# Optimization experiments

Measured on AMD Instinct MI355X. Metric: run time of the kernel, lower is better.

Reference implementation:

```python
import jax, jax.numpy as jnp
import numpy as np

N_NODES = 100000
N_EDGES = 800000
IN_FEAT = 64
HID_FEAT = 64
NUM_CLASS = 16


def _gcn_layer(H, src, dst, W, b, n_nodes):
    # Undirected aggregation: sum neighbor features in both edge directions,
    # plus self-loop, then linear transform.
    agg = (H
           + jax.ops.segment_sum(H[src], dst, num_segments=n_nodes)
           + jax.ops.segment_sum(H[dst], src, num_segments=n_nodes))
    return agg @ W + b


def setup_inputs() -> dict:
    key = jax.random.key(0)
    ks = jax.random.split(key, 8)
    X = jax.random.normal(ks[0], (N_NODES, IN_FEAT), dtype=jnp.float32)
    edge_list = jax.random.randint(ks[1], (2, N_EDGES), 0, N_NODES, dtype=jnp.int32)
    scale = 0.05
    W0 = jax.random.normal(ks[2], (IN_FEAT, HID_FEAT), dtype=jnp.float32) * scale
    W1 = jax.random.normal(ks[3], (HID_FEAT, HID_FEAT), dtype=jnp.float32) * scale
    W2 = jax.random.normal(ks[4], (HID_FEAT, HID_FEAT), dtype=jnp.float32) * scale
    W3 = jax.random.normal(ks[5], (HID_FEAT, NUM_CLASS), dtype=jnp.float32) * scale
    b0 = jnp.zeros((HID_FEAT,), jnp.float32)
    b1 = jnp.zeros((HID_FEAT,), jnp.float32)
    b2 = jnp.zeros((HID_FEAT,), jnp.float32)
    b3 = jnp.zeros((NUM_CLASS,), jnp.float32)
    return {"X": X, "edge_list": edge_list,
            "W0": W0, "b0": b0, "W1": W1, "b1": b1,
            "W2": W2, "b2": b2, "W3": W3, "b3": b3}


def reference(X, edge_list, W0, b0, W1, b1, W2, b2, W3, b3):
    n_nodes = X.shape[0]
    src, dst = edge_list[0], edge_list[1]
    # init layer + ReLU
    H = jax.nn.relu(_gcn_layer(X, src, dst, W0, b0, n_nodes))
    # 2 hidden layers + ReLU
    H = jax.nn.relu(_gcn_layer(H, src, dst, W1, b1, n_nodes))
    H = jax.nn.relu(_gcn_layer(H, src, dst, W2, b2, n_nodes))
    # output layer (no activation)
    H_out = _gcn_layer(H, src, dst, W3, b3, n_nodes)
    # global mean pooling over nodes -> [1, num_class]
    return jnp.mean(H_out, axis=0, keepdims=True)
```

## Files before the change

kernel.cpp:

```cpp
#include <hip/hip_runtime.h>

#define N_NODES 100000
#define N_EDGES 800000
#define SCAN_BLK 256
#define NB 391
#define NPB 256
#define CAP 5120
#define BIN_CAP 40
#define EDGES_PER_BLK 2048
#define BIN_GRID ((N_EDGES + EDGES_PER_BLK - 1) / EDGES_PER_BLK)

typedef unsigned int uint32;
typedef float f2x __attribute__((ext_vector_type(2)));

#if __has_builtin(__builtin_amdgcn_cvt_pk_f32_fp8) && __has_builtin(__builtin_amdgcn_cvt_pk_fp8_f32)
#define HW_FP8 1
#endif

__device__ __forceinline__ float fp8_dec_sw(uint32 v) {
    uint32 s = (v & 0x80u) << 24;
    uint32 e = (v >> 3) & 0xFu;
    uint32 m = v & 7u;
    if (e == 0) {
        float f = (float)m * 0.001953125f;
        return (v & 0x80u) ? -f : f;
    }
    return __uint_as_float(s | ((e + 120u) << 23) | (m << 20));
}
__device__ __forceinline__ uint32 fp8_enc_sw(float f) {
    uint32 u = __float_as_uint(f);
    uint32 s = (u >> 24) & 0x80u;
    uint32 a = u & 0x7FFFFFFFu;
    if (a < 0x3C000000u) {
        float af = __uint_as_float(a);
        uint32 m = (uint32)(af * 512.0f + 0.5f);
        if (m > 7u) return s | 0x08u;
        return s | m;
    }
    if (a >= 0x43E00000u) return s | 0x7Eu;
    uint32 r = a + 0x000FFFFFu + ((a >> 20) & 1u);
    uint32 e = (r >> 23) - 120u;
    uint32 m = (r >> 20) & 7u;
    if (e > 15u) return s | 0x7Eu;
    return s | (e << 3) | m;
}

__device__ __forceinline__ void dec4(uint32 v, float* o) {
#ifdef HW_FP8
    f2x lo = __builtin_amdgcn_cvt_pk_f32_fp8((int)v, false);
    f2x hi = __builtin_amdgcn_cvt_pk_f32_fp8((int)v, true);
    o[0] = lo.x; o[1] = lo.y; o[2] = hi.x; o[3] = hi.y;
#else
    o[0] = fp8_dec_sw(v); o[1] = fp8_dec_sw(v >> 8);
    o[2] = fp8_dec_sw(v >> 16); o[3] = fp8_dec_sw(v >> 24);
#endif
}
__device__ __forceinline__ uint32 enc4(float a, float b, float c, float d) {
#ifdef HW_FP8
    int v = 0;
    v = __builtin_amdgcn_cvt_pk_fp8_f32(a, b, v, false);
    v = __builtin_amdgcn_cvt_pk_fp8_f32(c, d, v, true);
    return (uint32)v;
#else
    return fp8_enc_sw(a) | (fp8_enc_sw(b) << 8) | (fp8_enc_sw(c) << 16) | (fp8_enc_sw(d) << 24);
#endif
}
__device__ __forceinline__ void acc16(uint4 h, float* a) {
    float t[16];
    dec4(h.x, t + 0); dec4(h.y, t + 4); dec4(h.z, t + 8); dec4(h.w, t + 12);
#pragma unroll
    for (int j = 0; j < 16; ++j) a[j] += t[j];
}

__global__ void f32_to_fp8_k(const float4* __restrict__ in, uint4* __restrict__ out, int n16) {
    int i = blockIdx.x * blockDim.x + threadIdx.x;
    if (i >= n16) return;
    float4 a = in[4 * i + 0];
    float4 b = in[4 * i + 1];
    float4 c = in[4 * i + 2];
    float4 d = in[4 * i + 3];
    uint4 o;
    o.x = enc4(a.x, a.y, a.z, a.w);
    o.y = enc4(b.x, b.y, b.z, b.w);
    o.z = enc4(c.x, c.y, c.z, c.w);
    o.w = enc4(d.x, d.y, d.z, d.w);
    out[i] = o;
}

__global__ void zero_int(int* __restrict__ p, int n) {
    int i = blockIdx.x * blockDim.x + threadIdx.x;
    if (i < n) p[i] = 0;
}

__global__ void zero_kernel(float* __restrict__ p, int n) {
    int i = blockIdx.x * blockDim.x + threadIdx.x;
    if (i < n) p[i] = 0.f;
}

__global__ void bin_kernel(const int* __restrict__ src, const int* __restrict__ dst,
                           int* __restrict__ bcnt, uint32* __restrict__ bpairs) {
    __shared__ int lcnt[NB];
    __shared__ uint32 lbin[NB * BIN_CAP];
    for (int b = threadIdx.x; b < NB; b += 256) lcnt[b] = 0;
    __syncthreads();

    int base = blockIdx.x * EDGES_PER_BLK;
#pragma unroll
    for (int j = 0; j < EDGES_PER_BLK / 256; ++j) {
        int e = base + j * 256 + threadIdx.x;
        if (e < N_EDGES) {
            int s = src[e], d = dst[e];
            {
                int b = d >> 8;
                uint32 val = ((uint32)(d & 255) << 17) | (uint32)s;
                int pos = atomicAdd(&lcnt[b], 1);
                if (pos < BIN_CAP) lbin[b * BIN_CAP + pos] = val;
                else {
                    int g = atomicAdd(&bcnt[b], 1);
                    if (g < CAP) bpairs[(size_t)b * CAP + g] = val;
                }
            }
            {
                int b = s >> 8;
                uint32 val = ((uint32)(s & 255) << 17) | (uint32)d;
                int pos = atomicAdd(&lcnt[b], 1);
                if (pos < BIN_CAP) lbin[b * BIN_CAP + pos] = val;
                else {
                    int g = atomicAdd(&bcnt[b], 1);
                    if (g < CAP) bpairs[(size_t)b * CAP + g] = val;
                }
            }
        }
    }
    __syncthreads();

    for (int b = threadIdx.x; b < NB; b += 256) {
        int k = lcnt[b];
        if (k > BIN_CAP) k = BIN_CAP;
        int g = 0;
        if (k > 0) g = atomicAdd(&bcnt[b], k);
        lcnt[b] = (g << 6) | k;
    }
    __syncthreads();
    const int TOT = NB * BIN_CAP;
    for (int idx = threadIdx.x; idx < TOT; idx += 256) {
        int b = idx / BIN_CAP;
        int j = idx - b * BIN_CAP;
        int pkv = lcnt[b];
        int k = pkv & 63;
        if (j < k) {
            int gg = (pkv >> 6) + j;
            if (gg < CAP) bpairs[(size_t)b * CAP + gg] = lbin[b * BIN_CAP + j];
        }
    }
}

__global__ void hist_kernel(const int* __restrict__ bcnt, const uint32* __restrict__ bpairs,
                            int* __restrict__ deg, int* __restrict__ partial) {
    __shared__ int h[NPB];
    int b = blockIdx.x;
    int t = threadIdx.x;
    h[t] = 0;
    __syncthreads();
    int cnt = bcnt[b];
    if (cnt > CAP) cnt = CAP;
    for (int i = t; i < cnt; i += 256)
        atomicAdd(&h[bpairs[(size_t)b * CAP + i] >> 17], 1);
    __syncthreads();
    int node = (b << 8) + t;
    int myh = h[t];
    if (node < N_NODES) deg[node] = myh;
    __syncthreads();
    for (int off = 128; off > 0; off >>= 1) {
        if (t < off) h[t] += h[t + off];
        __syncthreads();
    }
    if (t == 0) partial[b] = h[0];
}

__global__ void scan_tops(const int* __restrict__ partial, int* __restrict__ blockoff) {
    __shared__ int part[512];
    int t = threadIdx.x;
    part[t] = (t < NB) ? partial[t] : 0;
    __syncthreads();
    for (int off = 1; off < 512; off <<= 1) {
        int v = (t >= off) ? part[t - off] : 0;
        __syncthreads();
        part[t] += v;
        __syncthreads();
    }
    if (t < NB) blockoff[t] = (t == 0) ? 0 : part[t - 1];
}

__global__ void scan_apply(const int* __restrict__ deg, const int* __restrict__ blockoff,
                           int* __restrict__ rowptr) {
    __shared__ int part[SCAN_BLK];
    int t = threadIdx.x;
    int i = blockIdx.x * SCAN_BLK + t;
    int v = (i < N_NODES) ? deg[i] : 0;
    part[t] = v;
    __syncthreads();
    for (int off = 1; off < SCAN_BLK; off <<= 1) {
        int u = (t >= off) ? part[t - off] : 0;
        __syncthreads();
        part[t] += u;
        __syncthreads();
    }
    if (i < N_NODES) {
        int excl = blockoff[blockIdx.x] + part[t] - v;
        rowptr[i] = excl;
        if (i == N_NODES - 1) rowptr[N_NODES] = 2 * N_EDGES;
    }
}

__global__ void scatter_kernel(const int* __restrict__ bcnt, const uint32* __restrict__ bpairs,
                               const int* __restrict__ rowptr, int* __restrict__ adj) {
    __shared__ int lcur[NPB];
    __shared__ int stage[CAP];
    int b = blockIdx.x, t = threadIdx.x;
    int lo = b << 8;
    int base = rowptr[lo];
    int node = lo + t;
    lcur[t] = (node < N_NODES) ? (rowptr[node] - base) : 0;
    __syncthreads();
    int cnt = bcnt[b];
    if (cnt > CAP) cnt = CAP;
    for (int i = t; i < cnt; i += 256) {
        uint32 p = bpairs[(size_t)b * CAP + i];
        int ln = (int)(p >> 17);
        int nbr = (int)(p & 0x1FFFFu);
        int slot = atomicAdd(&lcur[ln], 1);
        if (slot < CAP) stage[slot] = nbr;
    }
    __syncthreads();
    for (int i = t; i < cnt; i += 256) adj[base + i] = stage[i];
}

#define FMA4(ACC, WV) ACC.x += a * (WV).x; ACC.y += a * (WV).y; \
                      ACC.z += a * (WV).z; ACC.w += a * (WV).w;
__global__ void __launch_bounds__(256)
fused_layer(const uint4* __restrict__ Hin,
            const int* __restrict__ rowptr,
            const int* __restrict__ adj,
            const float* __restrict__ W,
            const float* __restrict__ bias,
            uint4* __restrict__ Hout) {
    __shared__ uint4 aggL[64 * 5];

    int node_base = blockIdx.x * 64;
    {
        int n = node_base + (threadIdx.x >> 2);
        int c = threadIdx.x & 3;
        int ln = threadIdx.x >> 2;
        if (n < N_NODES) {
            int beg = rowptr[n], end = rowptr[n + 1];
            float a[16];
            uint4 s = Hin[(size_t)n * 4 + c];
            dec4(s.x, a + 0); dec4(s.y, a + 4); dec4(s.z, a + 8); dec4(s.w, a + 12);
            int i = beg;
            for (; i + 2 <= end; i += 2) {
                int v0 = adj[i];
                int v1 = adj[i + 1];
                uint4 h0 = Hin[(size_t)v0 * 4 + c];
                uint4 h1 = Hin[(size_t)v1 * 4 + c];
                acc16(h0, a);
                acc16(h1, a);
            }
            if (i < end) {
                uint4 h = Hin[(size_t)adj[i] * 4 + c];
                acc16(h, a);
            }
            uint4 o;
            o.x = enc4(a[0], a[1], a[2], a[3]);
            o.y = enc4(a[4], a[5], a[6], a[7]);
            o.z = enc4(a[8], a[9], a[10], a[11]);
            o.w = enc4(a[12], a[13], a[14], a[15]);
            aggL[ln * 5 + c] = o;
        }
    }
    __syncthreads();

    int ln2 = threadIdx.x & 63;
    int c2 = __builtin_amdgcn_readfirstlane(threadIdx.x >> 6);
    int n2 = node_base + ln2;
    if (n2 >= N_NODES) return;

    float4 acc0, acc1, acc2, acc3;
    {
        const float4* b4 = (const float4*)bias + c2 * 4;
        acc0 = b4[0]; acc1 = b4[1]; acc2 = b4[2]; acc3 = b4[3];
    }
    const float4* Wc = (const float4*)(W + c2 * 16);
#pragma unroll
    for (int q = 0; q < 4; ++q) {
        uint4 v = aggL[ln2 * 5 + q];
        float af[16];
        dec4(v.x, af + 0); dec4(v.y, af + 4); dec4(v.z, af + 8); dec4(v.w, af + 12);
#pragma unroll
        for (int k = 0; k < 16; ++k) {
            const float4* wr = Wc + (q * 16 + k) * 16;
            float a = af[k];
            float4 w0 = wr[0], w1 = wr[1], w2 = wr[2], w3 = wr[3];
            FMA4(acc0, w0)
            FMA4(acc1, w1)
            FMA4(acc2, w2)
            FMA4(acc3, w3)
        }
    }

    uint4 o;
    o.x = enc4(fmaxf(acc0.x, 0.f), fmaxf(acc0.y, 0.f), fmaxf(acc0.z, 0.f), fmaxf(acc0.w, 0.f));
    o.y = enc4(fmaxf(acc1.x, 0.f), fmaxf(acc1.y, 0.f), fmaxf(acc1.z, 0.f), fmaxf(acc1.w, 0.f));
    o.z = enc4(fmaxf(acc2.x, 0.f), fmaxf(acc2.y, 0.f), fmaxf(acc2.z, 0.f), fmaxf(acc2.w, 0.f));
    o.w = enc4(fmaxf(acc3.x, 0.f), fmaxf(acc3.y, 0.f), fmaxf(acc3.z, 0.f), fmaxf(acc3.w, 0.f));
    Hout[(size_t)n2 * 4 + c2] = o;
}

__global__ void wcolsum_fp8(const uint32* __restrict__ H32, const int* __restrict__ deg,
                            float* __restrict__ csum) {
    __shared__ float red[256];
    int f = threadIdx.x & 63;
    int r = threadIdx.x >> 6;
    int word = f >> 2;
    int sh = (f & 3) * 8;
    float local = 0.f;
    for (int n = blockIdx.x * 4 + r; n < N_NODES; n += gridDim.x * 4) {
        uint32 v = H32[(size_t)n * 16 + word];
        float h = fp8_dec_sw((v >> sh) & 0xFFu);
        local += (1.0f + (float)deg[n]) * h;
    }
    red[threadIdx.x] = local;
    __syncthreads();
    if (threadIdx.x < 64) {
        float s = red[threadIdx.x] + red[threadIdx.x + 64] +
                  red[threadIdx.x + 128] + red[threadIdx.x + 192];
        atomicAdd(&csum[f], s);
    }
}

__global__ void finalize_kernel(const float* __restrict__ csum,
                                const float* __restrict__ W3,
                                const float* __restrict__ b3,
                                float* __restrict__ out) {
    int j = threadIdx.x;
    if (j >= 16) return;
    const float inv = 1.0f / (float)N_NODES;
    float s = b3[j];
#pragma unroll
    for (int f = 0; f < 64; ++f) s += (csum[f] * inv) * W3[f * 16 + j];
    out[j] = s;
}

extern "C" void kernel_launch(void* const* d_in, const int* in_sizes, int n_in,
                              void* d_out, int out_size, void* d_ws, size_t ws_size,
                              hipStream_t stream) {
    const float* X  = (const float*)d_in[0];
    const int*   el = (const int*)d_in[1];
    const int*   src = el;
    const int*   dst = el + N_EDGES;
    const float* W0 = (const float*)d_in[2];
    const float* b0 = (const float*)d_in[3];
    const float* W1 = (const float*)d_in[4];
    const float* b1 = (const float*)d_in[5];
    const float* W2 = (const float*)d_in[6];
    const float* b2 = (const float*)d_in[7];
    const float* W3 = (const float*)d_in[8];
    const float* b3 = (const float*)d_in[9];
    float* out = (float*)d_out;

    uint32* Xb  = (uint32*)d_ws;
    uint32* B0  = Xb + (size_t)N_NODES * 16;
    uint32* B1  = B0 + (size_t)N_NODES * 16;
    float* csum = (float*)(B1 + (size_t)N_NODES * 16);
    int*   deg      = (int*)(csum + 64);
    int*   rowptr   = deg + N_NODES;
    int*   partial  = rowptr + N_NODES + 1;
    int*   blockoff = partial + NB;
    int*   bcnt     = blockoff + NB;
    uint32* bpairs  = (uint32*)(bcnt + NB);
    int*   adj      = (int*)(bpairs + (size_t)NB * CAP);

    const dim3 blk(256);
    const int convGrid  = (N_NODES * 4 + 255) / 256;
    const int layerGrid = (N_NODES * 4 + 255) / 256;

    f32_to_fp8_k<<<convGrid, blk, 0, stream>>>((const float4*)X, (uint4*)Xb, N_NODES * 4);

    zero_int<<<(NB + 255) / 256, blk, 0, stream>>>(bcnt, NB);
    bin_kernel<<<BIN_GRID, blk, 0, stream>>>(src, dst, bcnt, bpairs);
    hist_kernel<<<NB, blk, 0, stream>>>(bcnt, bpairs, deg, partial);
    scan_tops<<<1, 512, 0, stream>>>(partial, blockoff);
    scan_apply<<<NB, SCAN_BLK, 0, stream>>>(deg, blockoff, rowptr);
    scatter_kernel<<<NB, blk, 0, stream>>>(bcnt, bpairs, rowptr, adj);

    fused_layer<<<layerGrid, blk, 0, stream>>>((const uint4*)Xb, rowptr, adj, W0, b0, (uint4*)B0);
    fused_layer<<<layerGrid, blk, 0, stream>>>((const uint4*)B0, rowptr, adj, W1, b1, (uint4*)B1);
    fused_layer<<<layerGrid, blk, 0, stream>>>((const uint4*)B1, rowptr, adj, W2, b2, (uint4*)B0);

    zero_kernel<<<1, 64, 0, stream>>>(csum, 64);
    wcolsum_fp8<<<1024, blk, 0, stream>>>(B0, deg, csum);
    finalize_kernel<<<1, 64, 0, stream>>>(csum, W3, b3, out);
}
```

Before: 204.4 us.

## Fuse CSR histogram, scan and scatter into one bucket-build kernel

Replaces the hist, scan_tops, scan_apply and scatter kernels with a single per-bucket kernel. Each block computes its global base by summing the clamped bucket counts of all preceding buckets, builds a local histogram, scans it, writes rowptr and scatters adjacency through shared memory. It also merges the two zeroing kernels into one. This removes four launches and the global round trips for partial sums, at the cost of each block redundantly reading up to 391 bucket counts.

```diff
diff --git a/kernel.cpp b/kernel.cpp
--- a/kernel.cpp
+++ b/kernel.cpp
@@ -2,7 +2,6 @@
 
 #define N_NODES 100000
 #define N_EDGES 800000
-#define SCAN_BLK 256
 #define NB 391
 #define NPB 256
 #define CAP 5120
@@ -87,14 +86,10 @@
     out[i] = o;
 }
 
-__global__ void zero_int(int* __restrict__ p, int n) {
+__global__ void zero_misc(int* __restrict__ bcnt, float* __restrict__ csum) {
     int i = blockIdx.x * blockDim.x + threadIdx.x;
-    if (i < n) p[i] = 0;
-}
-
-__global__ void zero_kernel(float* __restrict__ p, int n) {
-    int i = blockIdx.x * blockDim.x + threadIdx.x;
-    if (i < n) p[i] = 0.f;
+    if (i < NB) bcnt[i] = 0;
+    if (i < 64) csum[i] = 0.f;
 }
 
 __global__ void bin_kernel(const int* __restrict__ src, const int* __restrict__ dst,
@@ -155,81 +150,61 @@
     }
 }
 
-__global__ void hist_kernel(const int* __restrict__ bcnt, const uint32* __restrict__ bpairs,
-                            int* __restrict__ deg, int* __restrict__ partial) {
+__global__ void __launch_bounds__(256)
+bucket_build(const int* __restrict__ bcnt, const uint32* __restrict__ bpairs,
+             int* __restrict__ deg, int* __restrict__ rowptr, int* __restrict__ adj) {
     __shared__ int h[NPB];
-    int b = blockIdx.x;
-    int t = threadIdx.x;
-    h[t] = 0;
-    __syncthreads();
+    __shared__ int part[NPB];
+    __shared__ int stage[CAP];
+    __shared__ int sbase;
+    int b = blockIdx.x, t = threadIdx.x;
+
+    {
+        int x = 0;
+        if (t < b) { int v = bcnt[t]; x = (v > CAP) ? CAP : v; }
+        int t2 = t + 256;
+        if (t2 < b) { int v = bcnt[t2]; x += (v > CAP) ? CAP : v; }
+        part[t] = x;
+        __syncthreads();
+        for (int off = 128; off > 0; off >>= 1) {
+            if (t < off) part[t] += part[t + off];
+            __syncthreads();
+        }
+        if (t == 0) sbase = part[0];
+        __syncthreads();
+    }
+    int base = sbase;
     int cnt = bcnt[b];
     if (cnt > CAP) cnt = CAP;
+
+    h[t] = 0;
+    __syncthreads();
     for (int i = t; i < cnt; i += 256)
         atomicAdd(&h[bpairs[(size_t)b * CAP + i] >> 17], 1);
     __syncthreads();
     int node = (b << 8) + t;
     int myh = h[t];
     if (node < N_NODES) deg[node] = myh;
-    __syncthreads();
-    for (int off = 128; off > 0; off >>= 1) {
-        if (t < off) h[t] += h[t + off];
-        __syncthreads();
-    }
-    if (t == 0) partial[b] = h[0];
-}
-
-__global__ void scan_tops(const int* __restrict__ partial, int* __restrict__ blockoff) {
-    __shared__ int part[512];
-    int t = threadIdx.x;
-    part[t] = (t < NB) ? partial[t] : 0;
-    __syncthreads();
-    for (int off = 1; off < 512; off <<= 1) {
-        int v = (t >= off) ? part[t - off] : 0;
-        __syncthreads();
-        part[t] += v;
-        __syncthreads();
-    }
-    if (t < NB) blockoff[t] = (t == 0) ? 0 : part[t - 1];
-}
-
-__global__ void scan_apply(const int* __restrict__ deg, const int* __restrict__ blockoff,
-                           int* __restrict__ rowptr) {
-    __shared__ int part[SCAN_BLK];
-    int t = threadIdx.x;
-    int i = blockIdx.x * SCAN_BLK + t;
-    int v = (i < N_NODES) ? deg[i] : 0;
-    part[t] = v;
-    __syncthreads();
-    for (int off = 1; off < SCAN_BLK; off <<= 1) {
+
+    part[t] = myh;
+    __syncthreads();
+    for (int off = 1; off < 256; off <<= 1) {
         int u = (t >= off) ? part[t - off] : 0;
         __syncthreads();
         part[t] += u;
         __syncthreads();
     }
-    if (i < N_NODES) {
-        int excl = blockoff[blockIdx.x] + part[t] - v;
-        rowptr[i] = excl;
-        if (i == N_NODES - 1) rowptr[N_NODES] = 2 * N_EDGES;
-    }
-}
-
-__global__ void scatter_kernel(const int* __restrict__ bcnt, const uint32* __restrict__ bpairs,
-                               const int* __restrict__ rowptr, int* __restrict__ adj) {
-    __shared__ int lcur[NPB];
-    __shared__ int stage[CAP];
-    int b = blockIdx.x, t = threadIdx.x;
-    int lo = b << 8;
-    int base = rowptr[lo];
-    int node = lo + t;
-    lcur[t] = (node < N_NODES) ? (rowptr[node] - base) : 0;
-    __syncthreads();
-    int cnt = bcnt[b];
-    if (cnt > CAP) cnt = CAP;
+    int excl = part[t] - myh;
+    if (node < N_NODES) rowptr[node] = base + excl;
+    if (node == N_NODES - 1) rowptr[N_NODES] = 2 * N_EDGES;
+
+    h[t] = excl;
+    __syncthreads();
     for (int i = t; i < cnt; i += 256) {
         uint32 p = bpairs[(size_t)b * CAP + i];
         int ln = (int)(p >> 17);
         int nbr = (int)(p & 0x1FFFFu);
-        int slot = atomicAdd(&lcur[ln], 1);
+        int slot = atomicAdd(&h[ln], 1);
         if (slot < CAP) stage[slot] = nbr;
     }
     __syncthreads();
@@ -374,9 +349,7 @@
     float* csum = (float*)(B1 + (size_t)N_NODES * 16);
     int*   deg      = (int*)(csum + 64);
     int*   rowptr   = deg + N_NODES;
-    int*   partial  = rowptr + N_NODES + 1;
-    int*   blockoff = partial + NB;
-    int*   bcnt     = blockoff + NB;
+    int*   bcnt     = rowptr + N_NODES + 1;
     uint32* bpairs  = (uint32*)(bcnt + NB);
     int*   adj      = (int*)(bpairs + (size_t)NB * CAP);
 
@@ -386,18 +359,14 @@
 
     f32_to_fp8_k<<<convGrid, blk, 0, stream>>>((const float4*)X, (uint4*)Xb, N_NODES * 4);
 
-    zero_int<<<(NB + 255) / 256, blk, 0, stream>>>(bcnt, NB);
+    zero_misc<<<(NB + 255) / 256, blk, 0, stream>>>(bcnt, csum);
     bin_kernel<<<BIN_GRID, blk, 0, stream>>>(src, dst, bcnt, bpairs);
-    hist_kernel<<<NB, blk, 0, stream>>>(bcnt, bpairs, deg, partial);
-    scan_tops<<<1, 512, 0, stream>>>(partial, blockoff);
-    scan_apply<<<NB, SCAN_BLK, 0, stream>>>(deg, blockoff, rowptr);
-    scatter_kernel<<<NB, blk, 0, stream>>>(bcnt, bpairs, rowptr, adj);
+    bucket_build<<<NB, blk, 0, stream>>>(bcnt, bpairs, deg, rowptr, adj);
 
     fused_layer<<<layerGrid, blk, 0, stream>>>((const uint4*)Xb, rowptr, adj, W0, b0, (uint4*)B0);
     fused_layer<<<layerGrid, blk, 0, stream>>>((const uint4*)B0, rowptr, adj, W1, b1, (uint4*)B1);
     fused_layer<<<layerGrid, blk, 0, stream>>>((const uint4*)B1, rowptr, adj, W2, b2, (uint4*)B0);
 
-    zero_kernel<<<1, 64, 0, stream>>>(csum, 64);
     wcolsum_fp8<<<1024, blk, 0, stream>>>(B0, deg, csum);
     finalize_kernel<<<1, 64, 0, stream>>>(csum, W3, b3, out);
 }
```

Measured after the change: 198.0 us. -3.1%, faster.
